# Kernel tuning notes

Measured on AMD Instinct MI355X. Metric: run time of the kernel, lower is better.

The kernel has to match this reference:

```python
import jax, jax.numpy as jnp
import numpy as np


def setup_inputs() -> dict:
    key = jax.random.key(0)
    k1, k2 = jax.random.split(key)
    B, N, M = 16, 4096, 4096
    x1 = jax.random.normal(k1, (B, N, 3), dtype=jnp.float32)
    x2 = jax.random.normal(k2, (B, M, 3), dtype=jnp.float32)
    return {"x1": x1, "x2": x2}


def reference(x1, x2) -> jnp.ndarray:
    # x1: [B, N, 3], x2: [B, M, 3]
    # dist_matrix[b, i, j] = ||x1[b,i] - x2[b,j]||^2 via |a|^2 + |b|^2 - 2 a.b
    x1_norm = jnp.sum(x1 * x1, axis=2, keepdims=True)           # [B, N, 1]
    x2_norm = jnp.sum(x2 * x2, axis=2)[:, None, :]              # [B, 1, M]
    cross = jnp.einsum('bnd,bmd->bnm', x1, x2)                  # [B, N, M]
    dist_matrix = x1_norm + x2_norm - 2.0 * cross               # [B, N, M]
    min_1_to_2 = jnp.min(dist_matrix, axis=2)                   # [B, N]
    min_2_to_1 = jnp.min(dist_matrix, axis=1)                   # [B, M]
    chamfer = jnp.mean(min_1_to_2, axis=1) + jnp.mean(min_2_to_1, axis=1)  # [B]
    return chamfer
```

## Files before the change

### kernel.cpp

```cpp
#include <hip/hip_runtime.h>


typedef __attribute__((ext_vector_type(8))) __bf16 bf16x8;
typedef __attribute__((ext_vector_type(16))) float f32x16;

#define PTS 4096
#define TILES 128
#define NB 16

__device__ __forceinline__ unsigned f2bf(float f) {
  unsigned u = __float_as_uint(f);
  return (u + 0x7FFFu + ((u >> 16) & 1u)) >> 16;
}
__device__ __forceinline__ float bf2f(unsigned s) {
  return __uint_as_float(s << 16);
}
__device__ __forceinline__ unsigned pk(unsigned lo, unsigned hi) {
  return (lo & 0xFFFFu) | (hi << 16);
}

__global__ __launch_bounds__(256) void prepack_b(const float* __restrict__ x1,
                                                 const float* __restrict__ x2,
                                                 uint4* __restrict__ Bfr,
                                                 unsigned* __restrict__ rowm) {
  const int id = blockIdx.x * 256 + threadIdx.x;
  rowm[id] = 0x7F800000u;
  const int d = id >> 16;
  const int b = (id >> 12) & (NB - 1);
  const int j = id & (PTS - 1);
  const float* q = (d ? x1 : x2) + (size_t)(b * PTS + j) * 3;
  const float x = q[0], y = q[1], z = q[2];
  const float sx = -2.f * x, sy = -2.f * y, sz = -2.f * z;
  const unsigned Hx = f2bf(sx), Hy = f2bf(sy), Hz = f2bf(sz);
  const unsigned Lx = f2bf(sx - bf2f(Hx));
  const unsigned Ly = f2bf(sy - bf2f(Hy));
  const unsigned Lz = f2bf(sz - bf2f(Hz));
  const float n = fmaf(x, x, fmaf(y, y, z * z));
  const unsigned nh = f2bf(n), nl = f2bf(n - bf2f(nh));
  const unsigned one = 0x3F80u;
  uint4 w0, w1;
  w0.x = pk(Hx, Hy); w0.y = pk(Hz, Lx); w0.z = pk(Ly, Lz); w0.w = pk(Hx, Hy);
  w1.x = pk(Hz, nh); w1.y = pk(nl, one); w1.z = pk(one, 0u); w1.w = 0u;
  uint4* base =
      Bfr + ((size_t)((d * NB + b) * TILES + (j >> 5)) * 2) * 32 + (j & 31);
  base[0]  = w0;
  base[32] = w1;
}

__global__ __launch_bounds__(256, 4) void chamfer_main(
    const float* __restrict__ x1, const float* __restrict__ x2,
    const uint4* __restrict__ Bfr, unsigned* __restrict__ rowm) {
  const int s  = blockIdx.x;
  const int d  = s & 1;
  const int b  = (s >> 1) & (NB - 1);
  const int ch = (s >> 5) & 1;
  const int rg = blockIdx.y;

  const int tid  = threadIdx.x;
  const int lane = tid & 63;
  const int half = lane >> 5;
  const int l31  = lane & 31;
  const int wave = tid >> 6;

  const float* P = d ? x2 : x1;
  const int t0 = rg * 8 + wave * 2;
  bf16x8 af[2];
#pragma unroll
  for (int rr = 0; rr < 2; ++rr) {
    const int r = (t0 + rr) * 32 + l31;
    const float* p = P + (size_t)(b * PTS + r) * 3;
    const float x = p[0], y = p[1], zc = p[2];
    const unsigned hx = f2bf(x), hy = f2bf(y), hz = f2bf(zc);
    const unsigned lx = f2bf(x - bf2f(hx));
    const unsigned ly = f2bf(y - bf2f(hy));
    const unsigned lz = f2bf(zc - bf2f(hz));
    const float n = fmaf(x, x, fmaf(y, y, zc * zc));
    const unsigned nh = f2bf(n), nl = f2bf(n - bf2f(nh));
    const unsigned one = 0x3F80u;
    uint4 w0, w1;
    w0.x = pk(hx, hy); w0.y = pk(hz, hx); w0.z = pk(hy, hz); w0.w = pk(lx, ly);
    w1.x = pk(lz, one); w1.y = pk(one, nh); w1.z = pk(nl, 0u); w1.w = 0u;
    uint4 w;
    w.x = half ? w1.x : w0.x; w.y = half ? w1.y : w0.y;
    w.z = half ? w1.z : w0.z; w.w = half ? w1.w : w0.w;
    af[rr] = *(const bf16x8*)&w;
  }
  const bf16x8 af0 = af[0], af1 = af[1];

  f32x16 zero;
#pragma unroll
  for (int e = 0; e < 16; ++e) zero[e] = 0.f;

  float rm0[16], rm1[16];
#pragma unroll
  for (int e = 0; e < 16; ++e) { rm0[e] = 3.0e38f; rm1[e] = 3.0e38f; }

  const uint4* bp = Bfr + ((size_t)((d * NB + b) * TILES + ch * 64) * 2) * 32;
  const int off = half * 32 + l31;
  bf16x8 buf[8];
#pragma unroll
  for (int t = 0; t < 4; ++t) buf[t] = *(const bf16x8*)&bp[t * 64 + off];

#pragma unroll 2
  for (int g = 0; g < 16; ++g) {
    const int cur = (g & 1) * 4;
    const int nxt = ((g + 1) & 1) * 4;
    const int pf  = ((g + 1) & 15) * 4;
#pragma unroll
    for (int t = 0; t < 4; ++t)
      buf[nxt + t] = *(const bf16x8*)&bp[(pf + t) * 64 + off];
#pragma unroll
    for (int t = 0; t < 4; t += 2) {
      const bf16x8 b0 = buf[cur + t], b1 = buf[cur + t + 1];
      const f32x16 a00 =
          __builtin_amdgcn_mfma_f32_32x32x16_bf16(af0, b0, zero, 0, 0, 0);
      const f32x16 a01 =
          __builtin_amdgcn_mfma_f32_32x32x16_bf16(af0, b1, zero, 0, 0, 0);
#pragma unroll
      for (int e = 0; e < 16; ++e)
        rm0[e] = fminf(fminf(a00[e], a01[e]), rm0[e]);
      const f32x16 a10 =
          __builtin_amdgcn_mfma_f32_32x32x16_bf16(af1, b0, zero, 0, 0, 0);
      const f32x16 a11 =
          __builtin_amdgcn_mfma_f32_32x32x16_bf16(af1, b1, zero, 0, 0, 0);
#pragma unroll
      for (int e = 0; e < 16; ++e)
        rm1[e] = fminf(fminf(a10[e], a11[e]), rm1[e]);
    }
  }

  unsigned* rbase = rowm + (size_t)(d * NB + b) * PTS + t0 * 32;
#pragma unroll
  for (int e = 0; e < 16; ++e) {
    float v = rm0[e];
    v = fminf(v, __shfl_xor(v, 1));
    v = fminf(v, __shfl_xor(v, 2));
    v = fminf(v, __shfl_xor(v, 4));
    v = fminf(v, __shfl_xor(v, 8));
    v = fminf(v, __shfl_xor(v, 16));
    if (l31 == e) {
      const int rl = (e & 3) + 8 * (e >> 2) + 4 * half;
      atomicMin(rbase + rl, __float_as_uint(fmaxf(v, 0.f)));
    }
  }
#pragma unroll
  for (int e = 0; e < 16; ++e) {
    float v = rm1[e];
    v = fminf(v, __shfl_xor(v, 1));
    v = fminf(v, __shfl_xor(v, 2));
    v = fminf(v, __shfl_xor(v, 4));
    v = fminf(v, __shfl_xor(v, 8));
    v = fminf(v, __shfl_xor(v, 16));
    if (l31 == e) {
      const int rl = 32 + (e & 3) + 8 * (e >> 2) + 4 * half;
      atomicMin(rbase + rl, __float_as_uint(fmaxf(v, 0.f)));
    }
  }
}

__global__ __launch_bounds__(256) void reduce_rows(
    const unsigned* __restrict__ rowm, float* __restrict__ out) {
  const int b = blockIdx.x;
  const int tid = threadIdx.x;
  const unsigned* r0 = rowm + (size_t)b * PTS;
  const unsigned* r1 = rowm + (size_t)(NB + b) * PTS;
  float s = 0.f;
  for (int i = tid; i < PTS; i += 256)
    s += __uint_as_float(r0[i]) + __uint_as_float(r1[i]);
  s += __shfl_xor(s, 1);
  s += __shfl_xor(s, 2);
  s += __shfl_xor(s, 4);
  s += __shfl_xor(s, 8);
  s += __shfl_xor(s, 16);
  s += __shfl_xor(s, 32);
  __shared__ float acc[4];
  if ((tid & 63) == 0) acc[tid >> 6] = s;
  __syncthreads();
  if (tid == 0) out[b] = (acc[0] + acc[1] + acc[2] + acc[3]) * (1.f / PTS);
}

extern "C" void kernel_launch(void* const* d_in, const int* in_sizes, int n_in,
                              void* d_out, int out_size, void* d_ws,
                              size_t ws_size, hipStream_t stream) {
  const float* x1 = (const float*)d_in[0];
  const float* x2 = (const float*)d_in[1];
  float* out = (float*)d_out;

  uint4* Bfr = (uint4*)d_ws;
  unsigned* rowm =
      (unsigned*)((char*)d_ws + (size_t)2 * NB * TILES * 2 * 32 * 16);

  prepack_b<<<(2 * NB * PTS) / 256, 256, 0, stream>>>(x1, x2, Bfr, rowm);
  dim3 grid(64, NB);
  chamfer_main<<<grid, 256, 0, stream>>>(x1, x2, Bfr, rowm);
  reduce_rows<<<NB, 256, 0, stream>>>(rowm, out);
}
```

Before: 88.26 us.

## Compute both min directions from a single distance-matrix pass with column-min partials

Instead of computing the distance matrix twice (once per direction), each block now computes one tile and extracts both row minima and column minima from the MFMA outputs. Column minima are reduced across halves by shuffle, then across waves through shared memory. Per-block partials are written without atomics, and a new reduce kernel combines row and column partials. This halves the MFMA work and the prepack work. In exchange it adds extra fmin and shuffle work per tile, shared-memory traffic, and lowers the occupancy hint to 3 blocks.

```diff
diff --git a/kernel.cpp b/kernel.cpp
--- a/kernel.cpp
+++ b/kernel.cpp
@@ -19,16 +19,14 @@
   return (lo & 0xFFFFu) | (hi << 16);
 }
 
-__global__ __launch_bounds__(256) void prepack_b(const float* __restrict__ x1,
-                                                 const float* __restrict__ x2,
+__global__ __launch_bounds__(256) void prepack_b(const float* __restrict__ x2,
                                                  uint4* __restrict__ Bfr,
-                                                 unsigned* __restrict__ rowm) {
+                                                 float* __restrict__ out) {
   const int id = blockIdx.x * 256 + threadIdx.x;
-  rowm[id] = 0x7F800000u;
-  const int d = id >> 16;
-  const int b = (id >> 12) & (NB - 1);
+  if (id < NB) out[id] = 0.f;
+  const int b = id >> 12;
   const int j = id & (PTS - 1);
-  const float* q = (d ? x1 : x2) + (size_t)(b * PTS + j) * 3;
+  const float* q = x2 + (size_t)(b * PTS + j) * 3;
   const float x = q[0], y = q[1], z = q[2];
   const float sx = -2.f * x, sy = -2.f * y, sz = -2.f * z;
   const unsigned Hx = f2bf(sx), Hy = f2bf(sy), Hz = f2bf(sz);
@@ -41,19 +39,17 @@
   uint4 w0, w1;
   w0.x = pk(Hx, Hy); w0.y = pk(Hz, Lx); w0.z = pk(Ly, Lz); w0.w = pk(Hx, Hy);
   w1.x = pk(Hz, nh); w1.y = pk(nl, one); w1.z = pk(one, 0u); w1.w = 0u;
-  uint4* base =
-      Bfr + ((size_t)((d * NB + b) * TILES + (j >> 5)) * 2) * 32 + (j & 31);
+  uint4* base = Bfr + ((size_t)(b * TILES + (j >> 5)) * 2) * 32 + (j & 31);
   base[0]  = w0;
   base[32] = w1;
 }
 
-__global__ __launch_bounds__(256, 4) void chamfer_main(
-    const float* __restrict__ x1, const float* __restrict__ x2,
-    const uint4* __restrict__ Bfr, unsigned* __restrict__ rowm) {
+__global__ __launch_bounds__(256, 3) void chamfer_main(
+    const float* __restrict__ x1, const uint4* __restrict__ Bfr,
+    float* __restrict__ rowpart, float* __restrict__ colpart) {
   const int s  = blockIdx.x;
-  const int d  = s & 1;
-  const int b  = (s >> 1) & (NB - 1);
-  const int ch = (s >> 5) & 1;
+  const int b  = s >> 2;
+  const int cq = s & 3;
   const int rg = blockIdx.y;
 
   const int tid  = threadIdx.x;
@@ -62,13 +58,14 @@
   const int l31  = lane & 31;
   const int wave = tid >> 6;
 
-  const float* P = d ? x2 : x1;
+  __shared__ float colw[4][1024];
+
   const int t0 = rg * 8 + wave * 2;
   bf16x8 af[2];
 #pragma unroll
   for (int rr = 0; rr < 2; ++rr) {
     const int r = (t0 + rr) * 32 + l31;
-    const float* p = P + (size_t)(b * PTS + r) * 3;
+    const float* p = x1 + (size_t)(b * PTS + r) * 3;
     const float x = p[0], y = p[1], zc = p[2];
     const unsigned hx = f2bf(x), hy = f2bf(y), hz = f2bf(zc);
     const unsigned lx = f2bf(x - bf2f(hx));
@@ -95,17 +92,17 @@
 #pragma unroll
   for (int e = 0; e < 16; ++e) { rm0[e] = 3.0e38f; rm1[e] = 3.0e38f; }
 
-  const uint4* bp = Bfr + ((size_t)((d * NB + b) * TILES + ch * 64) * 2) * 32;
+  const uint4* bp = Bfr + ((size_t)(b * TILES + cq * 32) * 2) * 32;
   const int off = half * 32 + l31;
   bf16x8 buf[8];
 #pragma unroll
   for (int t = 0; t < 4; ++t) buf[t] = *(const bf16x8*)&bp[t * 64 + off];
 
 #pragma unroll 2
-  for (int g = 0; g < 16; ++g) {
+  for (int g = 0; g < 8; ++g) {
     const int cur = (g & 1) * 4;
     const int nxt = ((g + 1) & 1) * 4;
-    const int pf  = ((g + 1) & 15) * 4;
+    const int pf  = ((g + 1) & 7) * 4;
 #pragma unroll
     for (int t = 0; t < 4; ++t)
       buf[nxt + t] = *(const bf16x8*)&bp[(pf + t) * 64 + off];
@@ -116,20 +113,37 @@
           __builtin_amdgcn_mfma_f32_32x32x16_bf16(af0, b0, zero, 0, 0, 0);
       const f32x16 a01 =
           __builtin_amdgcn_mfma_f32_32x32x16_bf16(af0, b1, zero, 0, 0, 0);
-#pragma unroll
-      for (int e = 0; e < 16; ++e)
-        rm0[e] = fminf(fminf(a00[e], a01[e]), rm0[e]);
       const f32x16 a10 =
           __builtin_amdgcn_mfma_f32_32x32x16_bf16(af1, b0, zero, 0, 0, 0);
       const f32x16 a11 =
           __builtin_amdgcn_mfma_f32_32x32x16_bf16(af1, b1, zero, 0, 0, 0);
 #pragma unroll
       for (int e = 0; e < 16; ++e)
+        rm0[e] = fminf(fminf(a00[e], a01[e]), rm0[e]);
+#pragma unroll
+      for (int e = 0; e < 16; ++e)
         rm1[e] = fminf(fminf(a10[e], a11[e]), rm1[e]);
+      float c0a = fminf(a00[0], a10[0]), c0b = fminf(a00[1], a10[1]);
+      float c1a = fminf(a01[0], a11[0]), c1b = fminf(a01[1], a11[1]);
+#pragma unroll
+      for (int e = 2; e < 16; e += 2) {
+        c0a = fminf(c0a, fminf(a00[e], a10[e]));
+        c0b = fminf(c0b, fminf(a00[e + 1], a10[e + 1]));
+        c1a = fminf(c1a, fminf(a01[e], a11[e]));
+        c1b = fminf(c1b, fminf(a01[e + 1], a11[e + 1]));
+      }
+      float c0 = fminf(c0a, c0b);
+      float c1 = fminf(c1a, c1b);
+      c0 = fminf(c0, __shfl_xor(c0, 32));
+      c1 = fminf(c1, __shfl_xor(c1, 32));
+      if (half == 0) {
+        colw[wave][(g * 4 + t) * 32 + l31]     = c0;
+        colw[wave][(g * 4 + t + 1) * 32 + l31] = c1;
+      }
     }
   }
 
-  unsigned* rbase = rowm + (size_t)(d * NB + b) * PTS + t0 * 32;
+  float* rb = rowpart + (size_t)(b * 4 + cq) * PTS + t0 * 32;
 #pragma unroll
   for (int e = 0; e < 16; ++e) {
     float v = rm0[e];
@@ -138,10 +152,7 @@
     v = fminf(v, __shfl_xor(v, 4));
     v = fminf(v, __shfl_xor(v, 8));
     v = fminf(v, __shfl_xor(v, 16));
-    if (l31 == e) {
-      const int rl = (e & 3) + 8 * (e >> 2) + 4 * half;
-      atomicMin(rbase + rl, __float_as_uint(fmaxf(v, 0.f)));
-    }
+    if (l31 == e) rb[(e & 3) + 8 * (e >> 2) + 4 * half] = v;
   }
 #pragma unroll
   for (int e = 0; e < 16; ++e) {
@@ -151,22 +162,36 @@
     v = fminf(v, __shfl_xor(v, 4));
     v = fminf(v, __shfl_xor(v, 8));
     v = fminf(v, __shfl_xor(v, 16));
-    if (l31 == e) {
-      const int rl = 32 + (e & 3) + 8 * (e >> 2) + 4 * half;
-      atomicMin(rbase + rl, __float_as_uint(fmaxf(v, 0.f)));
-    }
-  }
-}
-
-__global__ __launch_bounds__(256) void reduce_rows(
-    const unsigned* __restrict__ rowm, float* __restrict__ out) {
-  const int b = blockIdx.x;
+    if (l31 == e) rb[32 + (e & 3) + 8 * (e >> 2) + 4 * half] = v;
+  }
+
+  __syncthreads();
+  float* cb = colpart + (size_t)(b * 16 + rg) * PTS + cq * 1024;
+  for (int c = tid; c < 1024; c += 256)
+    cb[c] = fminf(fminf(colw[0][c], colw[1][c]),
+                  fminf(colw[2][c], colw[3][c]));
+}
+
+__global__ __launch_bounds__(256) void reduce_out(
+    const float* __restrict__ rowpart, const float* __restrict__ colpart,
+    float* __restrict__ out) {
+  const int b = blockIdx.x >> 2;
+  const int seg = blockIdx.x & 3;
   const int tid = threadIdx.x;
-  const unsigned* r0 = rowm + (size_t)b * PTS;
-  const unsigned* r1 = rowm + (size_t)(NB + b) * PTS;
   float s = 0.f;
-  for (int i = tid; i < PTS; i += 256)
-    s += __uint_as_float(r0[i]) + __uint_as_float(r1[i]);
+  const float* rp = rowpart + (size_t)b * 4 * PTS + seg * 1024;
+  for (int r = tid; r < 1024; r += 256) {
+    float m = fminf(fminf(rp[r], rp[PTS + r]),
+                    fminf(rp[2 * PTS + r], rp[3 * PTS + r]));
+    s += fmaxf(m, 0.f);
+  }
+  const float* cp = colpart + (size_t)b * 16 * PTS + seg * 1024;
+  for (int c = tid; c < 1024; c += 256) {
+    float m = cp[c];
+#pragma unroll
+    for (int k = 1; k < 16; ++k) m = fminf(m, cp[(size_t)k * PTS + c]);
+    s += fmaxf(m, 0.f);
+  }
   s += __shfl_xor(s, 1);
   s += __shfl_xor(s, 2);
   s += __shfl_xor(s, 4);
@@ -176,7 +201,8 @@
   __shared__ float acc[4];
   if ((tid & 63) == 0) acc[tid >> 6] = s;
   __syncthreads();
-  if (tid == 0) out[b] = (acc[0] + acc[1] + acc[2] + acc[3]) * (1.f / PTS);
+  if (tid == 0)
+    atomicAdd(&out[b], (acc[0] + acc[1] + acc[2] + acc[3]) * (1.f / PTS));
 }
 
 extern "C" void kernel_launch(void* const* d_in, const int* in_sizes, int n_in,
@@ -187,11 +213,11 @@
   float* out = (float*)d_out;
 
   uint4* Bfr = (uint4*)d_ws;
-  unsigned* rowm =
-      (unsigned*)((char*)d_ws + (size_t)2 * NB * TILES * 2 * 32 * 16);
-
-  prepack_b<<<(2 * NB * PTS) / 256, 256, 0, stream>>>(x1, x2, Bfr, rowm);
+  float* rowpart = (float*)((char*)d_ws + ((size_t)2 << 20));
+  float* colpart = (float*)((char*)d_ws + ((size_t)3 << 20));
+
+  prepack_b<<<(NB * PTS) / 256, 256, 0, stream>>>(x2, Bfr, out);
   dim3 grid(64, NB);
-  chamfer_main<<<grid, 256, 0, stream>>>(x1, x2, Bfr, rowm);
-  reduce_rows<<<NB, 256, 0, stream>>>(rowm, out);
-}
+  chamfer_main<<<grid, 256, 0, stream>>>(x1, Bfr, rowpart, colpart);
+  reduce_out<<<64, 256, 0, stream>>>(rowpart, colpart, out);
+}
```

After: 345.5 us. 3.91x slower.
